# Kernel optimization log

Measured on AMD Instinct MI355X. Metric: run time of the kernel, lower is better.

Reference implementation:

```python
import jax, jax.numpy as jnp
import numpy as np

# Model dims
D = 2048        # hidden_size
H = 16          # num_heads
KVH = 8         # num_key_value_heads
DH = 128        # head_dim
NUM_SLOTS = 16  # state-cache slots
B = 4           # prefill segments (regularized ragged batch)
L = 2048        # tokens per segment
T = B * L
C = 64          # GLA chunk size (fused_chunk_gla)
NEG = -1e30


def setup_inputs() -> dict:
    key = jax.random.key(0)
    k0, k1, k2, k3 = jax.random.split(key, 4)
    hidden_states = jax.random.normal(k0, (T, D), jnp.float32)
    W_qkv = jax.random.normal(k1, (D, (H + 2 * KVH) * DH), jnp.float32) * 0.02
    b_qkv = jnp.zeros(((H + 2 * KVH) * DH,), jnp.float32)
    kv_cache = jax.random.normal(k2, (NUM_SLOTS, H, DH, DH), jnp.float32) * 0.1
    state_indices = jax.random.randint(k3, (B,), 0, NUM_SLOTS, jnp.int32)
    return {"hidden_states": hidden_states, "W_qkv": W_qkv, "b_qkv": b_qkv,
            "kv_cache": kv_cache, "state_indices": state_indices}


def _to_chunks(x):
    # [T, H, d] -> [n_chunks, B, C, H, d]
    return x.reshape(B, L // C, C, H, DH).transpose(1, 0, 2, 3, 4)


def _gla_chunk_body(mask):
    def body(S, inp):
        # S: [B,H,dk,dv]; qc/kc/vc/gc: [B,C,H,d]
        qc, kc, vc, gc = inp
        Bc = jnp.cumsum(gc, axis=1)                       # inclusive log-decay within chunk
        # inter-chunk: initial state decayed by exp(Bc)
        o_inter = jnp.einsum('bchk,bhkv->bchv', qc * jnp.exp(Bc), S)
        # intra-chunk causal scores: A_ij = sum_d q_i,d * exp(B_i - B_j)_d * k_j,d, j<=i
        diff = Bc[:, :, None] - Bc[:, None, :]            # [B,Ci,Cj,H,dk], <=0 on lower tri
        diff = jnp.where(mask[None, :, :, None, None], diff, NEG)
        A = jnp.einsum('bihk,bijhk,bjhk->bijh', qc, jnp.exp(diff), kc)
        o = o_inter + jnp.einsum('bijh,bjhv->bihv', A, vc)
        # state update: S' = diag(exp(B_last)) S + sum_j (k_j exp(B_last - B_j)) v_j^T
        b_last = Bc[:, -1]                                # [B,H,dk]
        kg = kc * jnp.exp(b_last[:, None] - Bc)
        S_new = S * jnp.exp(b_last)[..., None] + jnp.einsum('bchk,bchv->bhkv', kg, vc)
        return S_new, o
    return jax.checkpoint(body)


def _forward(hidden_states, W_qkv, b_qkv, kv_cache, state_indices):
    qkv = hidden_states @ W_qkv + b_qkv
    q = qkv[:, :H * DH].reshape(T, H, DH)
    k = qkv[:, H * DH:(H + KVH) * DH].reshape(T, KVH, DH)
    v = qkv[:, (H + KVH) * DH:].reshape(T, KVH, DH)
    n_rep = H // KVH
    k = jnp.repeat(k, n_rep, axis=1)                      # repeat_kv (3D branch)
    v = jnp.repeat(v, n_rep, axis=1)
    q = jax.nn.relu(q) * DH ** -0.5                       # q_feature_map + fused_chunk_gla scale
    k = jnp.minimum(jax.nn.sigmoid(k), 0.95)              # sigmoid + clamp(max=clamp_max)
    g = jnp.log1p(-k)                                     # (1 - k).log()

    S0 = kv_cache[state_indices]                          # [B,H,dk,dv] per-slot initial states
    mask = jnp.tril(jnp.ones((C, C), bool))
    _, o = jax.lax.scan(_gla_chunk_body(mask), S0,
                        (_to_chunks(q), _to_chunks(k), _to_chunks(v), _to_chunks(g)))
    # [n_chunks,B,C,H,dv] -> per-segment concat [T, H*dv]
    return o.transpose(1, 0, 2, 3, 4).reshape(T, H * DH)


def reference(hidden_states, W_qkv, b_qkv, kv_cache, state_indices):
    return _forward(hidden_states, W_qkv, b_qkv, kv_cache, state_indices)
```

## Files before the change

kernel.cpp:

```cpp
#include <hip/hip_runtime.h>
#include <hip/hip_bf16.h>
#include <math.h>

#define RSQRT_DH 0.08838834764831845f

typedef __attribute__((ext_vector_type(8))) short short8;
typedef __attribute__((ext_vector_type(4))) float floatx4;

#define MFMA16(a, b, c) __builtin_amdgcn_mfma_f32_16x16x32_bf16((a), (b), (c), 0, 0, 0)

static __device__ __forceinline__ float bf2f(unsigned short u) {
  return __uint_as_float(((unsigned int)u) << 16);
}
static __device__ __forceinline__ unsigned short f2bf(float f) {
  unsigned int x = __float_as_uint(f);
  return (unsigned short)((x + 0x7fffu + ((x >> 16) & 1u)) >> 16);
}
static __device__ __forceinline__ ushort4 f4bf(float a, float b, float c, float d) {
  ushort4 r; r.x = f2bf(a); r.y = f2bf(b); r.z = f2bf(c); r.w = f2bf(d); return r;
}
static __device__ __forceinline__ short8 ld8u(const unsigned short* p) {
  short4 a = *(const short4*)p;
  short4 b = *(const short4*)(p + 4);
  short8 r;
  r[0] = a.x; r[1] = a.y; r[2] = a.z; r[3] = a.w;
  r[4] = b.x; r[5] = b.y; r[6] = b.z; r[7] = b.w;
  return r;
}

__launch_bounds__(256)
__global__ void k_cvt(const float* __restrict__ in, unsigned short* __restrict__ out, int n4) {
  int i = blockIdx.x * 256 + threadIdx.x;
  if (i >= n4) return;
  float4 v = ((const float4*)in)[i];
  ((ushort4*)out)[i] = f4bf(v.x, v.y, v.z, v.w);
}

__launch_bounds__(256)
__global__ void k_cvt_wt(const float* __restrict__ W, unsigned short* __restrict__ Wt) {
  __shared__ float tile[32][33];
  int t = threadIdx.x;
  int c = t & 31, r = t >> 5;
  int bx = blockIdx.x, by = blockIdx.y;
#pragma unroll
  for (int j = 0; j < 4; ++j)
    tile[r + j * 8][c] = W[(size_t)(by * 32 + r + j * 8) * 4096 + bx * 32 + c];
  __syncthreads();
#pragma unroll
  for (int j = 0; j < 4; ++j)
    Wt[(size_t)(bx * 32 + r + j * 8) * 2048 + by * 32 + c] = f2bf(tile[c][r + j * 8]);
}

__launch_bounds__(256, 4)
__global__ void k_gemm(const unsigned short* __restrict__ A,
                       const unsigned short* __restrict__ Bt,
                       const float* __restrict__ bias,
                       unsigned short* __restrict__ qb,
                       unsigned short* __restrict__ kb,
                       unsigned short* __restrict__ vb,
                       float* __restrict__ gf) {
  __shared__ unsigned short lds[16384];
  char* lb = (char*)lds;

  const int t = threadIdx.x;
  const int w = t >> 6, l = t & 63;
  const int wr = w >> 1, wc = w & 1;
  const int lr = l & 15, quad = l >> 4;

  const int id = blockIdx.x;
  const int x = id & 7, loc = id >> 3;
  const int bm = (x >> 1) * 16 + (loc >> 4);
  const int bn = (x & 1) * 16 + (loc & 15);
  const int m0 = bm * 128, n0 = bn * 128;

  const int srow = t >> 3;
  const int sslot = (t & 7) ^ (srow & 7);
  const unsigned short* agp = A + (size_t)(m0 + srow) * 2048 + sslot * 8;
  const unsigned short* bgp = Bt + (size_t)(n0 + srow) * 2048 + sslot * 8;

  const int c16_0 = ((quad) ^ (lr & 7)) * 16;
  const int c16_1 = ((4 + quad) ^ (lr & 7)) * 16;
  const char* pA = lb + wr * 8192 + lr * 128;
  const char* pB = lb + 16384 + wc * 8192 + lr * 128;

  floatx4 acc[4][4] = {};

  for (int kt = 0; kt < 32; ++kt) {
    __syncthreads();
#pragma unroll
    for (int it = 0; it < 4; ++it) {
      __builtin_amdgcn_global_load_lds(
          (const __attribute__((address_space(1))) void*)(agp + (size_t)it * 65536 + kt * 64),
          (__attribute__((address_space(3))) void*)(lb + it * 4096 + t * 16),
          16, 0, 0);
      __builtin_amdgcn_global_load_lds(
          (const __attribute__((address_space(1))) void*)(bgp + (size_t)it * 65536 + kt * 64),
          (__attribute__((address_space(3))) void*)(lb + 16384 + it * 4096 + t * 16),
          16, 0, 0);
    }
    __syncthreads();
#pragma unroll
    for (int ks = 0; ks < 2; ++ks) {
      const int c16 = ks ? c16_1 : c16_0;
      short8 af[4], bf[4];
#pragma unroll
      for (int i = 0; i < 4; ++i) af[i] = *(const short8*)(pA + i * 2048 + c16);
#pragma unroll
      for (int i = 0; i < 4; ++i) bf[i] = *(const short8*)(pB + i * 2048 + c16);
#pragma unroll
      for (int ti = 0; ti < 4; ++ti)
#pragma unroll
        for (int tj = 0; tj < 4; ++tj)
          acc[ti][tj] = MFMA16(af[ti], bf[tj], acc[ti][tj]);
    }
  }

  float* ldsf = (float*)lds;
  __syncthreads();

  const int c4 = (t & 31) * 4;
  float4 bv = *(const float4*)(bias + n0 + c4);

#pragma unroll
  for (int p = 0; p < 4; ++p) {
#pragma unroll
    for (int tj = 0; tj < 4; ++tj)
#pragma unroll
      for (int r = 0; r < 4; ++r)
        ldsf[(wr * 16 + quad * 4 + r) * 132 + wc * 64 + tj * 16 + lr] = acc[p][tj][r];
    __syncthreads();
#pragma unroll
    for (int it = 0; it < 4; ++it) {
      const int row32 = it * 8 + (t >> 5);
      const int grow = m0 + (row32 >> 4) * 64 + p * 16 + (row32 & 15);
      float4 f = *(const float4*)&ldsf[row32 * 132 + c4];
      f.x += bv.x; f.y += bv.y; f.z += bv.z; f.w += bv.w;
      if (n0 < 2048) {
        *(ushort4*)(qb + (size_t)grow * 2048 + n0 + c4) =
            f4bf(fmaxf(f.x, 0.f) * RSQRT_DH, fmaxf(f.y, 0.f) * RSQRT_DH,
                 fmaxf(f.z, 0.f) * RSQRT_DH, fmaxf(f.w, 0.f) * RSQRT_DH);
      } else if (n0 < 3072) {
        float sx = fminf(1.f / (1.f + __expf(-f.x)), 0.95f);
        float sy = fminf(1.f / (1.f + __expf(-f.y)), 0.95f);
        float sz = fminf(1.f / (1.f + __expf(-f.z)), 0.95f);
        float sw = fminf(1.f / (1.f + __expf(-f.w)), 0.95f);
        size_t idx = (size_t)grow * 1024 + (n0 - 2048) + c4;
        *(ushort4*)(kb + idx) = f4bf(sx, sy, sz, sw);
        float4 g4; g4.x = log1pf(-sx); g4.y = log1pf(-sy);
        g4.z = log1pf(-sz); g4.w = log1pf(-sw);
        *(float4*)(gf + idx) = g4;
      } else {
        *(ushort4*)(vb + (size_t)grow * 1024 + (n0 - 3072) + c4) =
            f4bf(f.x, f.y, f.z, f.w);
      }
    }
    __syncthreads();
  }
}

static __device__ __forceinline__ void scan64x128(float* sBc, int t) {
  float4* x4 = (float4*)sBc;
#pragma unroll
  for (int s = 1; s < 64; s <<= 1) {
    const int off = s * 32;
    float4 a[8];
#pragma unroll
    for (int j = 0; j < 8; ++j) {
      int e = j * 256 + t;
      if (e >= off) {
        float4 cu = x4[e];
        float4 pr = x4[e - off];
        a[j].x = cu.x + pr.x; a[j].y = cu.y + pr.y;
        a[j].z = cu.z + pr.z; a[j].w = cu.w + pr.w;
      }
    }
    __syncthreads();
#pragma unroll
    for (int j = 0; j < 8; ++j) {
      int e = j * 256 + t;
      if (e >= off) x4[e] = a[j];
    }
    __syncthreads();
  }
}

__launch_bounds__(256)
__global__ void k_phaseA(const unsigned short* __restrict__ kb,
                         const unsigned short* __restrict__ vb,
                         const float* __restrict__ gf,
                         float* __restrict__ blast,
                         unsigned short* __restrict__ Pb) {
  __shared__ float sBc[64 * 128];
  __shared__ float sKg[64 * 128];
  const int t = threadIdx.x;
  const int chunk = blockIdx.x, chain = blockIdx.y;
  const int b = chain >> 4, h = chain & 15, kvh = h >> 1;
  const int t0 = b * 2048 + chunk * 64;

#pragma unroll
  for (int rep = 0; rep < 8; ++rep) {
    int e = rep * 256 + t;
    int i = e >> 5, d4 = e & 31;
    *(float4*)(sBc + i * 128 + d4 * 4) =
        *(const float4*)(gf + (size_t)(t0 + i) * 1024 + kvh * 128 + d4 * 4);
  }
  __syncthreads();
  scan64x128(sBc, t);
  if (t < 128) blast[((size_t)chain * 32 + chunk) * 128 + t] = sBc[63 * 128 + t];
#pragma unroll
  for (int rep = 0; rep < 32; ++rep) {
    int e = rep * 256 + t;
    int i = e >> 7, d = e & 127;
    float kk = bf2f(kb[(size_t)(t0 + i) * 1024 + kvh * 128 + d]);
    sKg[e] = kk * __expf(sBc[63 * 128 + d] - sBc[e]);
  }
  __syncthreads();
  const int kq = t >> 3, vq = t & 7;
  const int kd0 = kq * 4, vd0 = vq * 16;
  float acc[4][16] = {};
  const unsigned short* vrow = vb + (size_t)t0 * 1024 + kvh * 128 + vd0;
  for (int i = 0; i < 64; ++i) {
    float4 kg4 = *(const float4*)(sKg + i * 128 + kd0);
    float ka[4] = {kg4.x, kg4.y, kg4.z, kg4.w};
    ushort4 v0 = *(const ushort4*)(vrow + (size_t)i * 1024);
    ushort4 v1 = *(const ushort4*)(vrow + (size_t)i * 1024 + 4);
    ushort4 v2 = *(const ushort4*)(vrow + (size_t)i * 1024 + 8);
    ushort4 v3 = *(const ushort4*)(vrow + (size_t)i * 1024 + 12);
    float vf[16] = {bf2f(v0.x), bf2f(v0.y), bf2f(v0.z), bf2f(v0.w),
                    bf2f(v1.x), bf2f(v1.y), bf2f(v1.z), bf2f(v1.w),
                    bf2f(v2.x), bf2f(v2.y), bf2f(v2.z), bf2f(v2.w),
                    bf2f(v3.x), bf2f(v3.y), bf2f(v3.z), bf2f(v3.w)};
#pragma unroll
    for (int r = 0; r < 4; ++r)
#pragma unroll
      for (int j = 0; j < 16; ++j) acc[r][j] += ka[r] * vf[j];
  }
  size_t pbase = ((size_t)chain * 32 + chunk) * 16384;
#pragma unroll
  for (int r = 0; r < 4; ++r)
#pragma unroll
    for (int j4 = 0; j4 < 4; ++j4)
      *(ushort4*)(Pb + pbase + (size_t)(kd0 + r) * 128 + vd0 + j4 * 4) =
          f4bf(acc[r][j4 * 4], acc[r][j4 * 4 + 1], acc[r][j4 * 4 + 2], acc[r][j4 * 4 + 3]);
}

__launch_bounds__(256)
__global__ void k_scan(const float* __restrict__ kv_cache,
                       const int* __restrict__ sidx,
                       const float* __restrict__ blast,
                       const unsigned short* __restrict__ Pb,
                       unsigned short* __restrict__ Sb) {
  const int t = threadIdx.x;
  const int part = blockIdx.x;
  const int chain = blockIdx.y;
  const int b = chain >> 4, h = chain & 15;
  const int e0 = part * 1024 + t * 4;
  const int kd = e0 >> 7;
  const int slot = sidx[b];
  float4 s = *(const float4*)(kv_cache + ((size_t)slot * 16 + h) * 16384 + e0);
#pragma unroll 1
  for (int c = 0; c < 32; ++c) {
    *(ushort4*)(Sb + ((size_t)c * 64 + chain) * 16384 + e0) = f4bf(s.x, s.y, s.z, s.w);
    float eb = __expf(blast[((size_t)chain * 32 + c) * 128 + kd]);
    ushort4 p = *(const ushort4*)(Pb + ((size_t)chain * 32 + c) * 16384 + e0);
    s.x = s.x * eb + bf2f(p.x);
    s.y = s.y * eb + bf2f(p.y);
    s.z = s.z * eb + bf2f(p.z);
    s.w = s.w * eb + bf2f(p.w);
  }
}

__launch_bounds__(256)
__global__ void k_output(const unsigned short* __restrict__ qb,
                         const unsigned short* __restrict__ kb,
                         const unsigned short* __restrict__ vb,
                         const float* __restrict__ gf,
                         const unsigned short* __restrict__ Sb,
                         float* __restrict__ out) {
  __shared__ float sBc[64 * 128];
  __shared__ unsigned short sR3[11136];
  unsigned short* sA   = sR3;
  unsigned short* sKE  = sR3 + 4608;
  unsigned short* sQE2 = sR3 + 4608 + 4352;
  unsigned short* sQE0 = sR3;
  unsigned short* sSt  = sR3 + 4608;
  unsigned short* sVt  = sR3 + 4608;

  const int t = threadIdx.x;
  const int w = t >> 6, l = t & 63;
  const int lr = l & 15, quad = l >> 4;
  const int chunk = blockIdx.x, chain = blockIdx.y;
  const int b = chain >> 4, h = chain & 15, kvh = h >> 1;
  const int t0 = b * 2048 + chunk * 64;
  const size_t sbase = ((size_t)chunk * 64 + chain) * 16384;

#pragma unroll
  for (int rep = 0; rep < 8; ++rep) {
    int e = rep * 256 + t, i = e >> 5, d4 = e & 31;
    *(float4*)(sBc + i * 128 + d4 * 4) =
        *(const float4*)(gf + (size_t)(t0 + i) * 1024 + kvh * 128 + d4 * 4);
  }
  __syncthreads();
  scan64x128(sBc, t);

  floatx4 o[8];
#pragma unroll
  for (int i = 0; i < 8; ++i) o[i] = 0.f;

#pragma unroll
  for (int kh = 0; kh < 2; ++kh) {
    __syncthreads();
#pragma unroll
    for (int rep = 0; rep < 2; ++rep) {
      int idx = rep * 256 + t;
      int i = idx >> 3, g = idx & 7;
      int k0 = kh * 64 + g * 8;
      short8 q8 = *(const short8*)(qb + (size_t)(t0 + i) * 2048 + h * 128 + k0);
      short8 r;
#pragma unroll
      for (int u = 0; u < 8; ++u)
        r[u] = (short)f2bf(bf2f((unsigned short)q8[u]) * __expf(sBc[i * 128 + k0 + u]));
      *(short8*)(sQE0 + i * 72 + g * 8) = r;
    }
#pragma unroll
    for (int vh = 0; vh < 2; ++vh) {
      __syncthreads();
#pragma unroll
      for (int rep = 0; rep < 2; ++rep) {
        int idx = rep * 256 + t;
        int kl = idx >> 3, g = idx & 7;
        short8 s8 = *(const short8*)(Sb + sbase + (size_t)(kh * 64 + kl) * 128 + vh * 64 + g * 8);
#pragma unroll
        for (int u = 0; u < 8; ++u) sSt[(g * 8 + u) * 76 + kl] = (unsigned short)s8[u];
      }
      __syncthreads();
      short8 af0 = *(const short8*)(sQE0 + (w * 16 + lr) * 72 + quad * 8);
      short8 af1 = *(const short8*)(sQE0 + (w * 16 + lr) * 72 + 32 + quad * 8);
#pragma unroll
      for (int tv = 0; tv < 4; ++tv) {
        const unsigned short* bp = sSt + (tv * 16 + lr) * 76 + quad * 8;
        short8 bf0 = ld8u(bp);
        short8 bf1 = ld8u(bp + 32);
        o[vh * 4 + tv] = MFMA16(af0, bf0, o[vh * 4 + tv]);
        o[vh * 4 + tv] = MFMA16(af1, bf1, o[vh * 4 + tv]);
      }
    }
  }

  __syncthreads();
  for (int idx = t; idx < 576; idx += 256)
    *(short8*)(sA + idx * 8) = (short8)0;
#pragma unroll
  for (int I = 0; I < 4; ++I) {
    const float* Rrow = (I > 0) ? (sBc + (I * 16 - 1) * 128) : nullptr;
    for (int base = 0; base < (I + 1) * 16; base += 32) {
      int nrows = min(32, (I + 1) * 16 - base);
      __syncthreads();
      int ngroups = nrows * 16;
      for (int idx = t; idx < ngroups; idx += 256) {
        int jl = idx >> 4, g = idx & 15;
        int j = base + jl, k0 = g * 8;
        short8 k8 = *(const short8*)(kb + (size_t)(t0 + j) * 1024 + kvh * 128 + k0);
        short8 r;
#pragma unroll
        for (int u = 0; u < 8; ++u) {
          int k = k0 + u;
          float Rk = Rrow ? Rrow[k] : 0.f;
          r[u] = (short)f2bf(bf2f((unsigned short)k8[u]) * __expf(Rk - sBc[j * 128 + k]));
        }
        *(short8*)(sKE + jl * 136 + k0) = r;
      }
      if (base == 0) {
        {
          int idx = t;
          int il = idx >> 4, g = idx & 15;
          int i = I * 16 + il, k0 = g * 8;
          short8 q8 = *(const short8*)(qb + (size_t)(t0 + i) * 2048 + h * 128 + k0);
          short8 r;
#pragma unroll
          for (int u = 0; u < 8; ++u) {
            int k = k0 + u;
            float Rk = Rrow ? Rrow[k] : 0.f;
            r[u] = (short)f2bf(bf2f((unsigned short)q8[u]) * __expf(sBc[i * 128 + k] - Rk));
          }
          *(short8*)(sQE2 + il * 136 + k0) = r;
        }
      }
      __syncthreads();
      const int J = w;
      if (J * 16 >= base && J * 16 < base + nrows) {
        floatx4 a4 = {};
#pragma unroll
        for (int ks = 0; ks < 4; ++ks) {
          short8 afr = *(const short8*)(sQE2 + lr * 136 + ks * 32 + quad * 8);
          short8 bfr = *(const short8*)(sKE + (J * 16 - base + lr) * 136 + ks * 32 + quad * 8);
          a4 = MFMA16(afr, bfr, a4);
        }
#pragma unroll
        for (int r = 0; r < 4; ++r) {
          int il = quad * 4 + r;
          float v = ((J < I) || (lr <= il)) ? a4[r] : 0.f;
          sA[(I * 16 + il) * 72 + J * 16 + lr] = f2bf(v);
        }
      }
    }
  }

  __syncthreads();
  short8 aA0 = *(const short8*)(sA + (w * 16 + lr) * 72 + quad * 8);
  short8 aA1 = *(const short8*)(sA + (w * 16 + lr) * 72 + 32 + quad * 8);
#pragma unroll
  for (int vh = 0; vh < 2; ++vh) {
    if (vh) __syncthreads();
#pragma unroll
    for (int rep = 0; rep < 2; ++rep) {
      int idx = rep * 256 + t;
      int j = idx >> 3, g = idx & 7;
      short8 v8 = *(const short8*)(vb + (size_t)(t0 + j) * 1024 + kvh * 128 + vh * 64 + g * 8);
#pragma unroll
      for (int u = 0; u < 8; ++u) sVt[(g * 8 + u) * 76 + j] = (unsigned short)v8[u];
    }
    __syncthreads();
#pragma unroll
    for (int tv = 0; tv < 4; ++tv) {
      const unsigned short* bp = sVt + (tv * 16 + lr) * 76 + quad * 8;
      short8 b0 = ld8u(bp);
      short8 b1 = ld8u(bp + 32);
      o[vh * 4 + tv] = MFMA16(aA0, b0, o[vh * 4 + tv]);
      o[vh * 4 + tv] = MFMA16(aA1, b1, o[vh * 4 + tv]);
    }
  }

#pragma unroll
  for (int tv8 = 0; tv8 < 8; ++tv8) {
    int col = (tv8 >> 2) * 64 + (tv8 & 3) * 16 + lr;
#pragma unroll
    for (int r = 0; r < 4; ++r) {
      int i = w * 16 + quad * 4 + r;
      out[(size_t)(t0 + i) * 2048 + h * 128 + col] = o[tv8][r];
    }
  }
}

extern "C" void kernel_launch(void* const* d_in, const int* in_sizes, int n_in,
                              void* d_out, int out_size, void* d_ws, size_t ws_size,
                              hipStream_t stream) {
  (void)in_sizes; (void)n_in; (void)out_size; (void)ws_size;
  const float* hs   = (const float*)d_in[0];
  const float* W    = (const float*)d_in[1];
  const float* bias = (const float*)d_in[2];
  const float* kvc  = (const float*)d_in[3];
  const int*   sidx = (const int*)d_in[4];

  char* ws = (char*)d_ws;
  unsigned short* Sb  = (unsigned short*)(ws + 0);
  unsigned short* hsb = (unsigned short*)(ws + 0);
  unsigned short* wtb = (unsigned short*)(ws + 33554432);
  unsigned short* qb  = (unsigned short*)(ws + 67108864);
  unsigned short* kb  = (unsigned short*)(ws + 100663296);
  unsigned short* vb  = (unsigned short*)(ws + 117440512);
  float*          gf  = (float*)(ws + 134217728);
  float*          bl  = (float*)(ws + 167772160);
  unsigned short* Pb  = (unsigned short*)d_out;
  float* out = (float*)d_out;

  k_cvt<<<dim3(16384), dim3(256), 0, stream>>>(hs, hsb, 16777216 / 4);
  k_cvt_wt<<<dim3(128, 64), dim3(256), 0, stream>>>(W, wtb);
  k_gemm<<<dim3(2048), dim3(256), 0, stream>>>(hsb, wtb, bias, qb, kb, vb, gf);
  k_phaseA<<<dim3(32, 64), dim3(256), 0, stream>>>(kb, vb, gf, bl, Pb);
  k_scan<<<dim3(16, 64), dim3(256), 0, stream>>>(kvc, sidx, bl, Pb, Sb);
  k_output<<<dim3(32, 64), dim3(256), 0, stream>>>(qb, kb, vb, gf, Sb, out);
}
```

Before: 563.4 us.

## Compute per-chunk KV outer-product state with bf16 MFMA in phase A

Replaces the scalar FP32 outer-product loop in k_phaseA, which builds the chunk's 128x128 Kg^T·V contribution, with bf16 MFMA 16x16x32 tiles. K-gated and V are staged transposed in padded LDS. The result is restaged through LDS and written to global memory as coalesced 16-byte rows. This removes most VALU FMA work and the strided uncoalesced V loads. In exchange the gated K is rounded to bf16 before the product rather than after, which adds a little precision loss.

After: 579.2 us. 1.03x slower.

```diff
diff --git a/kernel.cpp b/kernel.cpp
--- a/kernel.cpp
+++ b/kernel.cpp
@@ -191,8 +191,14 @@
                          float* __restrict__ blast,
                          unsigned short* __restrict__ Pb) {
   __shared__ float sBc[64 * 128];
-  __shared__ float sKg[64 * 128];
+  __shared__ __align__(16) unsigned short sT[2 * 128 * 76];
+  unsigned short* sKgT = sT;
+  unsigned short* sVT  = sT + 128 * 76;
+
   const int t = threadIdx.x;
+  const int w = t >> 6, l = t & 63;
+  const int lr = l & 15, quad = l >> 4;
+  const int wr = w >> 1, wc = w & 1;
   const int chunk = blockIdx.x, chain = blockIdx.y;
   const int b = chain >> 4, h = chain & 15, kvh = h >> 1;
   const int t0 = b * 2048 + chunk * 64;
@@ -207,41 +213,62 @@
   __syncthreads();
   scan64x128(sBc, t);
   if (t < 128) blast[((size_t)chain * 32 + chunk) * 128 + t] = sBc[63 * 128 + t];
-#pragma unroll
-  for (int rep = 0; rep < 32; ++rep) {
-    int e = rep * 256 + t;
-    int i = e >> 7, d = e & 127;
-    float kk = bf2f(kb[(size_t)(t0 + i) * 1024 + kvh * 128 + d]);
-    sKg[e] = kk * __expf(sBc[63 * 128 + d] - sBc[e]);
-  }
-  __syncthreads();
-  const int kq = t >> 3, vq = t & 7;
-  const int kd0 = kq * 4, vd0 = vq * 16;
-  float acc[4][16] = {};
-  const unsigned short* vrow = vb + (size_t)t0 * 1024 + kvh * 128 + vd0;
-  for (int i = 0; i < 64; ++i) {
-    float4 kg4 = *(const float4*)(sKg + i * 128 + kd0);
-    float ka[4] = {kg4.x, kg4.y, kg4.z, kg4.w};
-    ushort4 v0 = *(const ushort4*)(vrow + (size_t)i * 1024);
-    ushort4 v1 = *(const ushort4*)(vrow + (size_t)i * 1024 + 4);
-    ushort4 v2 = *(const ushort4*)(vrow + (size_t)i * 1024 + 8);
-    ushort4 v3 = *(const ushort4*)(vrow + (size_t)i * 1024 + 12);
-    float vf[16] = {bf2f(v0.x), bf2f(v0.y), bf2f(v0.z), bf2f(v0.w),
-                    bf2f(v1.x), bf2f(v1.y), bf2f(v1.z), bf2f(v1.w),
-                    bf2f(v2.x), bf2f(v2.y), bf2f(v2.z), bf2f(v2.w),
-                    bf2f(v3.x), bf2f(v3.y), bf2f(v3.z), bf2f(v3.w)};
-#pragma unroll
-    for (int r = 0; r < 4; ++r)
-#pragma unroll
-      for (int j = 0; j < 16; ++j) acc[r][j] += ka[r] * vf[j];
-  }
-  size_t pbase = ((size_t)chain * 32 + chunk) * 16384;
-#pragma unroll
-  for (int r = 0; r < 4; ++r)
-#pragma unroll
-    for (int j4 = 0; j4 < 4; ++j4)
-      *(ushort4*)(Pb + pbase + (size_t)(kd0 + r) * 128 + vd0 + j4 * 4) =
-          f4bf(acc[r][j4 * 4], acc[r][j4 * 4 + 1], acc[r][j4 * 4 + 2], acc[r][j4 * 4 + 3]);
+
+#pragma unroll
+  for (int rep = 0; rep < 4; ++rep) {
+    int idx = rep * 256 + t;
+    int i = idx >> 4, g = idx & 15;
+    int kd0 = g * 8;
+    short8 k8 = *(const short8*)(kb + (size_t)(t0 + i) * 1024 + kvh * 128 + kd0);
+    short8 v8 = *(const short8*)(vb + (size_t)(t0 + i) * 1024 + kvh * 128 + kd0);
+#pragma unroll
+    for (int u = 0; u < 8; ++u) {
+      int kd = kd0 + u;
+      float kg = bf2f((unsigned short)k8[u]) *
+                 __expf(sBc[63 * 128 + kd] - sBc[i * 128 + kd]);
+      sKgT[kd * 76 + i] = f2bf(kg);
+      sVT[kd * 76 + i] = (unsigned short)v8[u];
+    }
+  }
+  __syncthreads();
+
+  floatx4 acc[4][4] = {};
+#pragma unroll
+  for (int ks = 0; ks < 2; ++ks) {
+    short8 af[4], bf[4];
+#pragma unroll
+    for (int i2 = 0; i2 < 4; ++i2)
+      af[i2] = ld8u(sKgT + (wr * 64 + i2 * 16 + lr) * 76 + ks * 32 + quad * 8);
+#pragma unroll
+    for (int i2 = 0; i2 < 4; ++i2)
+      bf[i2] = ld8u(sVT + (wc * 64 + i2 * 16 + lr) * 76 + ks * 32 + quad * 8);
+#pragma unroll
+    for (int ti = 0; ti < 4; ++ti)
+#pragma unroll
+      for (int tj = 0; tj < 4; ++tj)
+        acc[ti][tj] = MFMA16(af[ti], bf[tj], acc[ti][tj]);
+  }
+
+  __syncthreads();
+  unsigned short* ps = sT;
+#pragma unroll
+  for (int ti = 0; ti < 4; ++ti)
+#pragma unroll
+    for (int tj = 0; tj < 4; ++tj)
+#pragma unroll
+      for (int r = 0; r < 4; ++r)
+        ps[(wr * 64 + ti * 16 + quad * 4 + r) * 136 + wc * 64 + tj * 16 + lr] =
+            f2bf(acc[ti][tj][r]);
+  __syncthreads();
+  const size_t pbase = ((size_t)chain * 32 + chunk) * 16384;
+  {
+    const int row = t >> 1, cb = (t & 1) * 64;
+    const unsigned short* src = ps + row * 136 + cb;
+    unsigned short* dst = Pb + pbase + row * 128 + cb;
+#pragma unroll
+    for (int j = 0; j < 8; ++j)
+      *(uint4*)(dst + j * 8) = *(const uint4*)(src + j * 8);
+  }
 }
 
 __launch_bounds__(256)
```
